# Optimization experiments

Measured on AMD Instinct MI355X. Metric: run time of the kernel, lower is better.

## Reference

```python
import jax, jax.numpy as jnp
import numpy as np

B, N, D_IN, D_OUT, H = 4, 2048, 1024, 1024, 16
HD = D_OUT // H

def _xavier(key, shape):
    fan_in, fan_out = shape[0], shape[1]
    a = jnp.sqrt(6.0 / (fan_in + fan_out))
    return jax.random.uniform(key, shape, jnp.float32, -a, a)

def setup_inputs() -> dict:
    key = jax.random.key(0)
    ks = jax.random.split(key, 6)
    x = jax.random.normal(ks[0], (B, N, D_IN), jnp.float32)
    w_q = _xavier(ks[1], (D_IN, D_OUT))
    w_k = _xavier(ks[2], (D_IN, D_OUT))
    w_v = _xavier(ks[3], (D_IN, D_OUT))
    # nn.Linear default init: uniform(-1/sqrt(fan_in), 1/sqrt(fan_in))
    bound = 1.0 / jnp.sqrt(D_OUT)
    w_o = jax.random.uniform(ks[4], (D_OUT, D_OUT), jnp.float32, -bound, bound)
    b_o = jax.random.uniform(ks[5], (D_OUT,), jnp.float32, -bound, bound)
    return {"x": x, "w_q": w_q, "w_k": w_k, "w_v": w_v, "w_o": w_o, "b_o": b_o}

def reference(x, w_q, w_k, w_v, w_o, b_o):
    b, n, _ = x.shape
    def split_heads(t):  # [b,n,D_OUT] -> [b,H,n,HD]
        return t.reshape(b, n, H, HD).transpose(0, 2, 1, 3)
    q = split_heads(x @ w_q)
    k = split_heads(x @ w_k)
    v = split_heads(x @ w_v)
    scores = jnp.einsum('bhqd,bhkd->bhqk', q, k) / jnp.sqrt(jnp.float32(HD))
    attn = jax.nn.softmax(scores, axis=-1)
    out = jnp.einsum('bhqk,bhkd->bhqd', attn, v)
    out = out.transpose(0, 2, 1, 3).reshape(b, n, D_OUT)
    return out @ w_o + b_o
```

## Files before the change

kernel.cpp:

```cpp
#include <hip/hip_runtime.h>
#include <stdint.h>
#include <stddef.h>

typedef __attribute__((ext_vector_type(8))) short bf16x8_t;
typedef __attribute__((ext_vector_type(4))) float f32x4_t;
typedef __attribute__((ext_vector_type(16))) float f32x16_t;
typedef __attribute__((ext_vector_type(4))) unsigned int u32x4_t;
typedef __attribute__((ext_vector_type(2))) unsigned int u32x2_t;

__device__ __forceinline__ unsigned short f2bf(float f) {
  union { float f; unsigned int u; } x; x.f = f;
  unsigned int r = x.u + 0x7fffu + ((x.u >> 16) & 1u);
  return (unsigned short)(r >> 16);
}

__device__ __forceinline__ float e2(float x) { return __builtin_amdgcn_exp2f(x); }

__device__ __forceinline__ unsigned int cvtpk(float lo, float hi) {
  unsigned int d;
  asm("v_cvt_pk_bf16_f32 %0, %1, %2" : "=v"(d) : "v"(lo), "v"(hi));
  return d;
}
__device__ __forceinline__ void plswap(unsigned int& a, unsigned int& b) {
  asm("v_permlane32_swap_b32 %0, %1" : "+v"(a), "+v"(b));
}

__device__ __forceinline__ void gload16(const void* g, void* l) {
  __builtin_amdgcn_global_load_lds(
      (const __attribute__((address_space(1))) void*)g,
      (__attribute__((address_space(3))) void*)l, 16, 0, 0);
}

#define QSCALE 0.18033688011112042f

__global__ __launch_bounds__(256)
void f32_to_bf16(const float* __restrict__ in, unsigned short* __restrict__ out) {
  size_t i = ((size_t)blockIdx.x * 256 + threadIdx.x) * 8;
  f32x4_t a = *(const f32x4_t*)(in + i);
  f32x4_t b = *(const f32x4_t*)(in + i + 4);
  bf16x8_t o;
#pragma unroll
  for (int j = 0; j < 4; ++j) { o[j] = (short)f2bf(a[j]); o[j + 4] = (short)f2bf(b[j]); }
  *(bf16x8_t*)(out + i) = o;
}

__global__ __launch_bounds__(256)
void transpose_cvt3(const float* __restrict__ w0, const float* __restrict__ w1,
                    const float* __restrict__ w2, unsigned short* __restrict__ out) {
  __shared__ float t[32][33];
  const float* in = blockIdx.z == 0 ? w0 : (blockIdx.z == 1 ? w1 : w2);
  unsigned short* o = out + (size_t)blockIdx.z * 1024 * 1024;
  const int x = threadIdx.x & 31, y = threadIdx.x >> 5;
  const int bx = blockIdx.x * 32, by = blockIdx.y * 32;
#pragma unroll
  for (int i = 0; i < 32; i += 8)
    t[y + i][x] = in[(size_t)(by + y + i) * 1024 + bx + x];
  __syncthreads();
#pragma unroll
  for (int i = 0; i < 32; i += 8)
    o[(size_t)(bx + y + i) * 1024 + by + x] = f2bf(t[x][y + i]);
}

__global__ __launch_bounds__(256)
void transpose_cvt(const float* __restrict__ in, unsigned short* __restrict__ out) {
  __shared__ float t[32][33];
  const int x = threadIdx.x & 31, y = threadIdx.x >> 5;
  const int bx = blockIdx.x * 32, by = blockIdx.y * 32;
#pragma unroll
  for (int i = 0; i < 32; i += 8)
    t[y + i][x] = in[(size_t)(by + y + i) * 1024 + bx + x];
  __syncthreads();
#pragma unroll
  for (int i = 0; i < 32; i += 8)
    out[(size_t)(bx + y + i) * 1024 + by + x] = f2bf(t[x][y + i]);
}

__global__ __launch_bounds__(256)
void transpose_v(const unsigned short* __restrict__ in, unsigned short* __restrict__ out) {
  __shared__ unsigned short t[64][65];
  const int bh = blockIdx.y;
  const int n0 = blockIdx.x * 64;
  const int c = threadIdx.x & 63, r4 = threadIdx.x >> 6;
#pragma unroll
  for (int i = 0; i < 64; i += 4)
    t[r4 + i][c] = in[((size_t)bh * 2048 + n0 + r4 + i) * 64 + c];
  __syncthreads();
#pragma unroll
  for (int i = 0; i < 64; i += 4)
    out[((size_t)bh * 64 + r4 + i) * 2048 + n0 + c] = t[c][r4 + i];
}

template <int MODE>
__global__ __launch_bounds__(256, 2)
void gemm128(const unsigned short* __restrict__ A,
             const unsigned short* __restrict__ Bt,
             void* __restrict__ Cv,
             const float* __restrict__ bias,
             int M, int K, int Nn) {
  constexpr int BK = 32;
  __shared__ __align__(16) unsigned short As[128 * BK];
  __shared__ __align__(16) unsigned short Bs[128 * BK];

  const int tid = threadIdx.x;
  const int wave = tid >> 6;
  const int lane = tid & 63;
  const int l15 = lane & 15;
  const int lq = lane >> 4;
  const int row0 = blockIdx.x * 128;
  const int col0 = blockIdx.y * 128;
  const int wr = (wave >> 1) * 64;
  const int wc = (wave & 1) * 64;

  f32x4_t acc[4][4];
#pragma unroll
  for (int m = 0; m < 4; ++m)
#pragma unroll
    for (int n = 0; n < 4; ++n) acc[m][n] = (f32x4_t)0.f;

  const int p0 = tid, p1 = tid + 256;
  const int pr0 = p0 >> 2, ps0 = (p0 & 3) ^ (pr0 & 3);
  const int pr1 = p1 >> 2, ps1 = (p1 & 3) ^ (pr1 & 3);

  char* As0 = (char*)As + wave * 1024;
  char* As1 = (char*)As + 4096 + wave * 1024;
  char* Bs0 = (char*)Bs + wave * 1024;
  char* Bs1 = (char*)Bs + 4096 + wave * 1024;

  const unsigned short* Ap0 = A + (size_t)(row0 + pr0) * K + ps0 * 8;
  const unsigned short* Ap1 = A + (size_t)(row0 + pr1) * K + ps1 * 8;
  const unsigned short* Bp0 = Bt + (size_t)(col0 + pr0) * K + ps0 * 8;
  const unsigned short* Bp1 = Bt + (size_t)(col0 + pr1) * K + ps1 * 8;

  for (int k0 = 0; k0 < K; k0 += BK) {
    __syncthreads();
    gload16(Ap0 + k0, As0);
    gload16(Ap1 + k0, As1);
    gload16(Bp0 + k0, Bs0);
    gload16(Bp1 + k0, Bs1);
    __syncthreads();

    bf16x8_t af[4], bfr[4];
#pragma unroll
    for (int m = 0; m < 4; ++m) {
      int r = wr + m * 16 + l15;
      af[m] = *(const bf16x8_t*)((const char*)As + r * 64 + ((lq ^ (r & 3)) << 4));
    }
#pragma unroll
    for (int n = 0; n < 4; ++n) {
      int c = wc + n * 16 + l15;
      bfr[n] = *(const bf16x8_t*)((const char*)Bs + c * 64 + ((lq ^ (c & 3)) << 4));
    }
#pragma unroll
    for (int m = 0; m < 4; ++m)
#pragma unroll
      for (int n = 0; n < 4; ++n)
        acc[m][n] = __builtin_amdgcn_mfma_f32_16x16x32_bf16(af[m], bfr[n], acc[m][n], 0, 0, 0);
  }

#pragma unroll
  for (int m = 0; m < 4; ++m) {
    int rb = row0 + wr + m * 16 + lq * 4;
#pragma unroll
    for (int n = 0; n < 4; ++n) {
      int col = col0 + wc + n * 16 + l15;
#pragma unroll
      for (int j = 0; j < 4; ++j) {
        int row = rb + j;
        float v = acc[m][n][j];
        if constexpr (MODE == 0) {
          int which = col >> 10, cl = col & 1023;
          int b = row >> 11, nn = row & 2047, h = cl >> 6, hd = cl & 63;
          float s = (which == 0) ? QSCALE : 1.0f;
          ((unsigned short*)Cv)[(size_t)which * 8388608 +
                                (((size_t)(b * 16 + h)) * 2048 + nn) * 64 + hd] = f2bf(v * s);
        } else {
          ((float*)Cv)[(size_t)row * Nn + col] = v + bias[col];
        }
      }
    }
  }
}

__global__ __launch_bounds__(256, 2)
void attn_mfma(const unsigned short* __restrict__ qb,
               const unsigned short* __restrict__ kb,
               const unsigned short* __restrict__ vtb,
               unsigned short* __restrict__ ab) {
  __shared__ __align__(16) unsigned short Ks[2][8192];
  __shared__ __align__(16) unsigned short Vs[2][8192];

  const int tid = threadIdx.x, wave = tid >> 6, lane = tid & 63;
  const int l31 = lane & 31, hi = lane >> 5;

  const int bid = blockIdx.x;
  const int xcd = bid & 7, w = bid >> 3;
  const int bh = xcd * 8 + (w >> 4);
  const int q0 = (w & 15) * 128;

  const unsigned short* qrow = qb + ((size_t)bh * 2048 + q0 + wave * 32 + l31) * 64;
  bf16x8_t qf[4];
#pragma unroll
  for (int ks = 0; ks < 4; ++ks)
    qf[ks] = *(const bf16x8_t*)(qrow + ks * 16 + hi * 8);

  f32x16_t O[2];
#pragma unroll
  for (int hb = 0; hb < 2; ++hb) O[hb] = (f32x16_t)0.f;
  float m_run = -1e30f, l_run = 0.f;

  const unsigned short* kbase = kb + (size_t)bh * 2048 * 64;
  const unsigned short* vbase = vtb + (size_t)bh * 64 * 2048;
  int koff[4], voff[4];
#pragma unroll
  for (int i = 0; i < 4; ++i) {
    int c = tid + 256 * i;
    int kr = c >> 3, kp = c & 7, kl = kp ^ (kr & 7);
    koff[i] = kr * 64 + kl * 8;
    int vr = c >> 4, vp = c & 15, vl = (vp & 8) | ((vp & 7) ^ (vr & 7));
    voff[i] = vr * 2048 + vl * 8;
  }

#pragma unroll
  for (int i = 0; i < 4; ++i) {
    gload16(kbase + koff[i], (char*)Ks[0] + (tid + 256 * i) * 16);
    gload16(vbase + voff[i], (char*)Vs[0] + (tid + 256 * i) * 16);
  }
  __syncthreads();

  for (int t = 0; t < 16; ++t) {
    const int cur = t & 1;
    if (t < 15) {
      const unsigned short* kt = kbase + (size_t)(t + 1) * 8192;
      const unsigned short* vt = vbase + (t + 1) * 128;
#pragma unroll
      for (int i = 0; i < 4; ++i) {
        gload16(kt + koff[i], (char*)Ks[cur ^ 1] + (tid + 256 * i) * 16);
        gload16(vt + voff[i], (char*)Vs[cur ^ 1] + (tid + 256 * i) * 16);
      }
    }
    const char* Kc = (const char*)Ks[cur];
    const char* Vc = (const char*)Vs[cur];

    f32x16_t sacc[4];
#pragma unroll
    for (int kbk = 0; kbk < 4; ++kbk) sacc[kbk] = (f32x16_t)0.f;
#pragma unroll
    for (int kbk = 0; kbk < 4; ++kbk) {
#pragma unroll
      for (int ks = 0; ks < 4; ++ks) {
        int key = kbk * 32 + l31;
        bf16x8_t kf = *(const bf16x8_t*)(Kc + key * 128 + (((ks * 2 + hi) ^ (key & 7)) << 4));
        sacc[kbk] = __builtin_amdgcn_mfma_f32_32x32x16_bf16(kf, qf[ks], sacc[kbk], 0, 0, 0);
      }
    }

    float mx = -1e30f;
#pragma unroll
    for (int kbk = 0; kbk < 4; ++kbk)
#pragma unroll
      for (int r = 0; r < 16; ++r) mx = fmaxf(mx, sacc[kbk][r]);
    mx = fmaxf(mx, __shfl_xor(mx, 32));

    const float mn = fmaxf(m_run, mx);
    const float alpha = e2(m_run - mn);
    m_run = mn;
#pragma unroll
    for (int hb = 0; hb < 2; ++hb)
#pragma unroll
      for (int r = 0; r < 16; ++r) O[hb][r] *= alpha;

    float psum = 0.f;
#pragma unroll
    for (int kbk = 0; kbk < 4; ++kbk) {
      float p[16];
#pragma unroll
      for (int r = 0; r < 16; ++r) {
        p[r] = e2(sacc[kbk][r] - mn);
        psum += p[r];
      }
#pragma unroll
      for (int u = 0; u < 2; ++u) {
        unsigned int a0 = cvtpk(p[8 * u + 0], p[8 * u + 1]);
        unsigned int b0 = cvtpk(p[8 * u + 4], p[8 * u + 5]);
        plswap(a0, b0);
        unsigned int a1 = cvtpk(p[8 * u + 2], p[8 * u + 3]);
        unsigned int b1 = cvtpk(p[8 * u + 6], p[8 * u + 7]);
        plswap(a1, b1);
        u32x4_t fw; fw[0] = a0; fw[1] = a1; fw[2] = b0; fw[3] = b1;
        bf16x8_t pfrag = *(bf16x8_t*)&fw;
        const int ks2 = kbk * 2 + u;
#pragma unroll
        for (int hb = 0; hb < 2; ++hb) {
          int hd = hb * 32 + l31;
          int sl = ks2 * 2 + hi;
          bf16x8_t vf = *(const bf16x8_t*)(Vc + hd * 256 +
                          (((sl & 8) | ((sl & 7) ^ (hd & 7))) << 4));
          O[hb] = __builtin_amdgcn_mfma_f32_32x32x16_bf16(vf, pfrag, O[hb], 0, 0, 0);
        }
      }
    }
    psum += __shfl_xor(psum, 32);
    l_run = l_run * alpha + psum;

    __syncthreads();
  }

  const int b = bh >> 4, h = bh & 15;
  const float inv = 1.f / l_run;
  const int row = q0 + wave * 32 + l31;
  unsigned short* op = ab + ((size_t)(b * 2048 + row)) * 1024 + h * 64;
#pragma unroll
  for (int hb = 0; hb < 2; ++hb)
#pragma unroll
    for (int tt = 0; tt < 4; ++tt) {
      u32x2_t d;
      d[0] = cvtpk(O[hb][4 * tt + 0] * inv, O[hb][4 * tt + 1] * inv);
      d[1] = cvtpk(O[hb][4 * tt + 2] * inv, O[hb][4 * tt + 3] * inv);
      *(u32x2_t*)(op + hb * 32 + tt * 8 + hi * 4) = d;
    }
}

extern "C" void kernel_launch(void* const* d_in, const int* in_sizes, int n_in,
                              void* d_out, int out_size, void* d_ws, size_t ws_size,
                              hipStream_t stream) {
  const float* x  = (const float*)d_in[0];
  const float* wq = (const float*)d_in[1];
  const float* wk = (const float*)d_in[2];
  const float* wv = (const float*)d_in[3];
  const float* wo = (const float*)d_in[4];
  const float* bo = (const float*)d_in[5];
  float* out = (float*)d_out;

  const size_t MB = 1ull << 20;
  char* ws = (char*)d_ws;
  unsigned short* xb  = (unsigned short*)(ws);
  unsigned short* ab  = xb;
  unsigned short* qkv = (unsigned short*)(ws + 17 * MB);
  unsigned short* vtb = (unsigned short*)(ws + 68 * MB);
  unsigned short* wT  = (unsigned short*)(ws + 85 * MB);
  unsigned short* woT = (unsigned short*)(ws + 91 * MB);

  const size_t X = 8388608;

  const dim3 tb(256);
  f32_to_bf16<<<4096, tb, 0, stream>>>(x, xb);
  transpose_cvt3<<<dim3(32, 32, 3), tb, 0, stream>>>(wq, wk, wv, wT);
  transpose_cvt<<<dim3(32, 32), tb, 0, stream>>>(wo, woT);

  gemm128<0><<<dim3(64, 24), tb, 0, stream>>>(xb, wT, (void*)qkv, nullptr, 8192, 1024, 3072);

  transpose_v<<<dim3(32, 64), tb, 0, stream>>>(qkv + 2 * X, vtb);

  attn_mfma<<<dim3(1024), tb, 0, stream>>>(qkv, qkv + X, vtb, ab);

  gemm128<1><<<dim3(64, 8), tb, 0, stream>>>(ab, woT, (void*)out, bo, 8192, 1024, 1024);
}
```

Baseline: 280.4 us.

## Double-buffer GEMM LDS, remap blocks per XCD, widen attention blocks to 512 threads

The GEMM now double-buffers its LDS tiles, so the next K-slice is loaded while MFMAs run on the current one. Its 2D grid becomes a 1D grid with an XCD-aware tile mapping to improve L2 locality, and it declares occupancy 3. The attention kernel moves to 512-thread blocks covering 256 query rows, so each K/V tile staged in LDS is shared by twice as many waves. The softmax running-sum update is also reordered. LDS use doubles in the GEMM and register pressure rises with the new launch bounds.

```diff
diff --git a/kernel.cpp b/kernel.cpp
--- a/kernel.cpp
+++ b/kernel.cpp
@@ -91,23 +91,27 @@
 }
 
 template <int MODE>
-__global__ __launch_bounds__(256, 2)
+__global__ __launch_bounds__(256, 3)
 void gemm128(const unsigned short* __restrict__ A,
              const unsigned short* __restrict__ Bt,
              void* __restrict__ Cv,
              const float* __restrict__ bias,
              int M, int K, int Nn) {
   constexpr int BK = 32;
-  __shared__ __align__(16) unsigned short As[128 * BK];
-  __shared__ __align__(16) unsigned short Bs[128 * BK];
+  __shared__ __align__(16) unsigned short As[2][128 * BK];
+  __shared__ __align__(16) unsigned short Bs[2][128 * BK];
 
   const int tid = threadIdx.x;
   const int wave = tid >> 6;
   const int lane = tid & 63;
   const int l15 = lane & 15;
   const int lq = lane >> 4;
-  const int row0 = blockIdx.x * 128;
-  const int col0 = blockIdx.y * 128;
+
+  const int bid = blockIdx.x;
+  const int xcd = bid & 7, tt = bid >> 3;
+  const int row0 = (xcd * 8 + (tt & 7)) * 128;
+  const int col0 = (tt >> 3) * 128;
+
   const int wr = (wave >> 1) * 64;
   const int wc = (wave & 1) * 64;
 
@@ -120,41 +124,55 @@
   const int p0 = tid, p1 = tid + 256;
   const int pr0 = p0 >> 2, ps0 = (p0 & 3) ^ (pr0 & 3);
   const int pr1 = p1 >> 2, ps1 = (p1 & 3) ^ (pr1 & 3);
-
-  char* As0 = (char*)As + wave * 1024;
-  char* As1 = (char*)As + 4096 + wave * 1024;
-  char* Bs0 = (char*)Bs + wave * 1024;
-  char* Bs1 = (char*)Bs + 4096 + wave * 1024;
 
   const unsigned short* Ap0 = A + (size_t)(row0 + pr0) * K + ps0 * 8;
   const unsigned short* Ap1 = A + (size_t)(row0 + pr1) * K + ps1 * 8;
   const unsigned short* Bp0 = Bt + (size_t)(col0 + pr0) * K + ps0 * 8;
   const unsigned short* Bp1 = Bt + (size_t)(col0 + pr1) * K + ps1 * 8;
 
-  for (int k0 = 0; k0 < K; k0 += BK) {
-    __syncthreads();
-    gload16(Ap0 + k0, As0);
-    gload16(Ap1 + k0, As1);
-    gload16(Bp0 + k0, Bs0);
-    gload16(Bp1 + k0, Bs1);
-    __syncthreads();
-
+  {
+    char* ab = (char*)As[0];
+    char* bb = (char*)Bs[0];
+    gload16(Ap0, ab + p0 * 16);
+    gload16(Ap1, ab + p1 * 16);
+    gload16(Bp0, bb + p0 * 16);
+    gload16(Bp1, bb + p1 * 16);
+  }
+  __syncthreads();
+
+  const int NIT = K / BK;
+  for (int it = 0; it < NIT; ++it) {
+    const int cur = it & 1;
+    if (it + 1 < NIT) {
+      const int k0n = (it + 1) * BK;
+      char* ab = (char*)As[cur ^ 1];
+      char* bb = (char*)Bs[cur ^ 1];
+      gload16(Ap0 + k0n, ab + p0 * 16);
+      gload16(Ap1 + k0n, ab + p1 * 16);
+      gload16(Bp0 + k0n, bb + p0 * 16);
+      gload16(Bp1 + k0n, bb + p1 * 16);
+    }
+
+    const char* Ac = (const char*)As[cur];
+    const char* Bc = (const char*)Bs[cur];
     bf16x8_t af[4], bfr[4];
 #pragma unroll
     for (int m = 0; m < 4; ++m) {
       int r = wr + m * 16 + l15;
-      af[m] = *(const bf16x8_t*)((const char*)As + r * 64 + ((lq ^ (r & 3)) << 4));
+      af[m] = *(const bf16x8_t*)(Ac + r * 64 + ((lq ^ (r & 3)) << 4));
     }
 #pragma unroll
     for (int n = 0; n < 4; ++n) {
       int c = wc + n * 16 + l15;
-      bfr[n] = *(const bf16x8_t*)((const char*)Bs + c * 64 + ((lq ^ (c & 3)) << 4));
+      bfr[n] = *(const bf16x8_t*)(Bc + c * 64 + ((lq ^ (c & 3)) << 4));
     }
 #pragma unroll
     for (int m = 0; m < 4; ++m)
 #pragma unroll
       for (int n = 0; n < 4; ++n)
         acc[m][n] = __builtin_amdgcn_mfma_f32_16x16x32_bf16(af[m], bfr[n], acc[m][n], 0, 0, 0);
+
+    __syncthreads();
   }
 
 #pragma unroll
@@ -181,7 +199,7 @@
   }
 }
 
-__global__ __launch_bounds__(256, 2)
+__global__ __launch_bounds__(512, 4)
 void attn_mfma(const unsigned short* __restrict__ qb,
                const unsigned short* __restrict__ kb,
                const unsigned short* __restrict__ vtb,
@@ -194,8 +212,8 @@
 
   const int bid = blockIdx.x;
   const int xcd = bid & 7, w = bid >> 3;
-  const int bh = xcd * 8 + (w >> 4);
-  const int q0 = (w & 15) * 128;
+  const int bh = xcd * 8 + (w >> 3);
+  const int q0 = (w & 7) * 256;
 
   const unsigned short* qrow = qb + ((size_t)bh * 2048 + q0 + wave * 32 + l31) * 64;
   bf16x8_t qf[4];
@@ -210,10 +228,10 @@
 
   const unsigned short* kbase = kb + (size_t)bh * 2048 * 64;
   const unsigned short* vbase = vtb + (size_t)bh * 64 * 2048;
-  int koff[4], voff[4];
-#pragma unroll
-  for (int i = 0; i < 4; ++i) {
-    int c = tid + 256 * i;
+  int koff[2], voff[2];
+#pragma unroll
+  for (int i = 0; i < 2; ++i) {
+    int c = tid + 512 * i;
     int kr = c >> 3, kp = c & 7, kl = kp ^ (kr & 7);
     koff[i] = kr * 64 + kl * 8;
     int vr = c >> 4, vp = c & 15, vl = (vp & 8) | ((vp & 7) ^ (vr & 7));
@@ -221,9 +239,9 @@
   }
 
 #pragma unroll
-  for (int i = 0; i < 4; ++i) {
-    gload16(kbase + koff[i], (char*)Ks[0] + (tid + 256 * i) * 16);
-    gload16(vbase + voff[i], (char*)Vs[0] + (tid + 256 * i) * 16);
+  for (int i = 0; i < 2; ++i) {
+    gload16(kbase + koff[i], (char*)Ks[0] + (tid + 512 * i) * 16);
+    gload16(vbase + voff[i], (char*)Vs[0] + (tid + 512 * i) * 16);
   }
   __syncthreads();
 
@@ -233,9 +251,9 @@
       const unsigned short* kt = kbase + (size_t)(t + 1) * 8192;
       const unsigned short* vt = vbase + (t + 1) * 128;
 #pragma unroll
-      for (int i = 0; i < 4; ++i) {
-        gload16(kt + koff[i], (char*)Ks[cur ^ 1] + (tid + 256 * i) * 16);
-        gload16(vt + voff[i], (char*)Vs[cur ^ 1] + (tid + 256 * i) * 16);
+      for (int i = 0; i < 2; ++i) {
+        gload16(kt + koff[i], (char*)Ks[cur ^ 1] + (tid + 512 * i) * 16);
+        gload16(vt + voff[i], (char*)Vs[cur ^ 1] + (tid + 512 * i) * 16);
       }
     }
     const char* Kc = (const char*)Ks[cur];
@@ -264,6 +282,7 @@
     const float mn = fmaxf(m_run, mx);
     const float alpha = e2(m_run - mn);
     m_run = mn;
+    l_run *= alpha;
 #pragma unroll
     for (int hb = 0; hb < 2; ++hb)
 #pragma unroll
@@ -275,7 +294,7 @@
       float p[16];
 #pragma unroll
       for (int r = 0; r < 16; ++r) {
-        p[r] = e2(sacc[kbk][r] - mn);
+        p[r] = e2(sacc[kbk][r] - m_run);
         psum += p[r];
       }
 #pragma unroll
@@ -300,7 +319,7 @@
       }
     }
     psum += __shfl_xor(psum, 32);
-    l_run = l_run * alpha + psum;
+    l_run += psum;
 
     __syncthreads();
   }
@@ -347,11 +366,11 @@
   transpose_cvt3<<<dim3(32, 32, 3), tb, 0, stream>>>(wq, wk, wv, wT);
   transpose_cvt<<<dim3(32, 32), tb, 0, stream>>>(wo, woT);
 
-  gemm128<0><<<dim3(64, 24), tb, 0, stream>>>(xb, wT, (void*)qkv, nullptr, 8192, 1024, 3072);
+  gemm128<0><<<dim3(1536), tb, 0, stream>>>(xb, wT, (void*)qkv, nullptr, 8192, 1024, 3072);
 
   transpose_v<<<dim3(32, 64), tb, 0, stream>>>(qkv + 2 * X, vtb);
 
-  attn_mfma<<<dim3(1024), tb, 0, stream>>>(qkv, qkv + X, vtb, ab);
-
-  gemm128<1><<<dim3(64, 8), tb, 0, stream>>>(ab, woT, (void*)out, bo, 8192, 1024, 1024);
-}
+  attn_mfma<<<dim3(512), dim3(512), 0, stream>>>(qkv, qkv + X, vtb, ab);
+
+  gemm128<1><<<dim3(512), tb, 0, stream>>>(ab, woT, (void*)out, bo, 8192, 1024, 1024);
+}
```

Result: slower. 291.8 us (+4.1%).
